# Performance work log

Hardware: AMD Instinct MI355X
Metric: run time of the kernel (lower is better)

## Reference

```python
import jax, jax.numpy as jnp
import numpy as np

HEADS = 8
CPH = 32


def _rel_pos_indices(h, w):
    # same construction as the torch buffer, done statically in numpy
    coords = np.stack(np.meshgrid(np.arange(h), np.arange(w), indexing='ij')).reshape(2, -1)  # [2, N]
    rel = coords[:, :, None] - coords[:, None, :]  # [2, N, N]
    idx = (rel[0] + h - 1) * (2 * w - 1) + (rel[1] + w - 1)  # [N, N]
    return jnp.asarray(idx, dtype=jnp.int32)


def setup_inputs() -> dict:
    key = jax.random.key(0)
    ks = jax.random.split(key, 6)
    B, C, H, W = 2, 256, 48, 48
    emb = HEADS * CPH  # 256
    x = jax.random.normal(ks[0], (B, C, H, W), dtype=jnp.float32)
    # GDN params (kept positive so sqrt is well-defined)
    gdn_beta = jnp.ones((C,), dtype=jnp.float32)
    gdn_gamma = 0.1 * jnp.eye(C, dtype=jnp.float32) + 0.001 * jax.random.uniform(ks[1], (C, C), dtype=jnp.float32)
    w_qkv = 0.02 * jax.random.normal(ks[2], (3 * emb, C), dtype=jnp.float32)
    w_out = 0.02 * jax.random.normal(ks[3], (C, emb), dtype=jnp.float32)
    b_out = jnp.zeros((C,), dtype=jnp.float32)
    table_size = (2 * H - 1) * (2 * W - 1)
    rel_bias_table = 0.02 * jax.random.normal(ks[4], (table_size, HEADS), dtype=jnp.float32)
    return {"x": x, "gdn_beta": gdn_beta, "gdn_gamma": gdn_gamma,
            "w_qkv": w_qkv, "w_out": w_out, "b_out": b_out,
            "rel_bias_table": rel_bias_table}


def reference(x, gdn_beta, gdn_gamma, w_qkv, w_out, b_out, rel_bias_table):
    B, C, H, W = x.shape
    N = H * W
    emb = HEADS * CPH
    scale = CPH ** (-0.5)

    # GDN: y = x / sqrt(beta + gamma * x^2)  (1x1 conv over channels of x^2)
    norm = jnp.einsum('bchw,dc->bdhw', x * x, gdn_gamma) + gdn_beta[None, :, None, None]
    xn = x / jnp.sqrt(norm)

    # flatten spatial, channels last: [B, N, C]
    t = xn.reshape(B, C, N).transpose(0, 2, 1)

    # qkv projection (no bias)
    qkv = (t @ w_qkv.T).reshape(B, N, 3, HEADS, CPH).transpose(2, 0, 3, 1, 4)  # [3, B, h, N, d]
    q, k, v = qkv[0], qkv[1], qkv[2]

    attn = jnp.einsum('bhnd,bhmd->bhnm', q, k) * scale  # [B, h, N, N]

    # gathered relative position bias: [h, N, N]
    idx = _rel_pos_indices(H, W)  # [N, N], static ints
    bias = rel_bias_table[idx.reshape(-1)].reshape(N, N, HEADS).transpose(2, 0, 1)
    attn = jax.nn.softmax(attn + bias[None], axis=-1)

    # NOTE: faithful to the original quirk — reshape (B, h, N, d) directly
    # to (B, N, C) with NO head/seq transpose, exactly like the torch code.
    res = jnp.einsum('bhnm,bhmd->bhnd', attn, v).reshape(B, N, emb)

    out = res @ w_out.T + b_out  # [B, N, C]
    return out.transpose(0, 2, 1).reshape(B, C, H, W)
```

## Files before the change

kernel.cpp:

```cpp
#include <hip/hip_runtime.h>
#include <cstdint>
#include <cstddef>

typedef __attribute__((ext_vector_type(8))) short short8;
typedef __attribute__((ext_vector_type(4))) float floatx4;
typedef __attribute__((ext_vector_type(4))) unsigned short ushort4v;

#define NB 2
#define NPIX 2304
#define TBL 9025
#define TBLP 9032
#define L2E 1.4426950408889634f
#define QSCALE 0.17677669529663689f

__device__ __forceinline__ float b2f(unsigned short u) {
  union { unsigned int i; float f; } v; v.i = ((unsigned int)u) << 16; return v.f;
}
__device__ __forceinline__ unsigned short f2b(float f) {
  union { float f; unsigned int i; } v; v.f = f;
  return (unsigned short)((v.i + 0x7fffu + ((v.i >> 16) & 1u)) >> 16);
}
__device__ __forceinline__ unsigned short f2b_fast(float f) {
  union { float f; unsigned int i; } v; v.f = f;
  return (unsigned short)((v.i + 0x8000u) >> 16);
}

__global__ __launch_bounds__(256) void prep_k(
    const float* __restrict__ gamma, const float* __restrict__ wqkv,
    const float* __restrict__ wout, const float* __restrict__ table,
    unsigned short* __restrict__ gb, unsigned short* __restrict__ qb,
    unsigned short* __restrict__ wb, float* __restrict__ tbf)
{
  int i = blockIdx.x * 256 + threadIdx.x;
  if (i < 65536)  gb[i] = f2b(gamma[i]);
  if (i < 196608) qb[i] = f2b(wqkv[i]);
  if (i < 65536)  wb[i] = f2b(wout[i]);
  if (i < TBL * 8) {
    int e = i >> 3, h = i & 7;
    tbf[(size_t)h * TBLP + e] = table[i] * L2E;
  }
}

template<int MODE>
__global__ __launch_bounds__(256) void gemm_k(
    const unsigned short* __restrict__ A,
    const void* __restrict__ Bv,
    const float* __restrict__ vec,
    unsigned short* __restrict__ o0,
    unsigned short* __restrict__ o1,
    unsigned short* __restrict__ o2,
    float* __restrict__ of)
{
  __shared__ unsigned short Al[64][40];
  __shared__ unsigned short Bl[64][40];
  const float* __restrict__ X = (const float*)Bv;
  const unsigned short* __restrict__ Bw = (const unsigned short*)Bv;

  const int n0 = blockIdx.x * 64;
  const int m0 = blockIdx.y * 64;
  const int b  = blockIdx.z;
  const int tid = threadIdx.x;
  const int wave = tid >> 6, lane = tid & 63;
  const int wm = wave >> 1, wn = wave & 1;
  const int lm = lane & 15, quad = lane >> 4;

  floatx4 acc[2][2] = {};

  for (int k0 = 0; k0 < 256; k0 += 32) {
    __syncthreads();
    {
      int ml = tid >> 2, ko = (tid & 3) * 8;
      *(short8*)&Al[ml][ko] = *(const short8*)&A[(size_t)(m0 + ml) * 256 + k0 + ko];
    }
    if (MODE == 0) {
      int kk = tid >> 3, n8 = (tid & 7) * 8;
      const float* xr = &X[((size_t)(b * 256 + k0 + kk)) * NPIX + n0 + n8];
      float4 x0 = *(const float4*)xr;
      float4 x1 = *(const float4*)(xr + 4);
      Bl[n8 + 0][kk] = f2b(x0.x * x0.x);
      Bl[n8 + 1][kk] = f2b(x0.y * x0.y);
      Bl[n8 + 2][kk] = f2b(x0.z * x0.z);
      Bl[n8 + 3][kk] = f2b(x0.w * x0.w);
      Bl[n8 + 4][kk] = f2b(x1.x * x1.x);
      Bl[n8 + 5][kk] = f2b(x1.y * x1.y);
      Bl[n8 + 6][kk] = f2b(x1.z * x1.z);
      Bl[n8 + 7][kk] = f2b(x1.w * x1.w);
    } else {
      int nl = tid >> 2, ko = (tid & 3) * 8;
      short8 bv = *(const short8*)&Bw[((size_t)b * NPIX + n0 + nl) * 256 + k0 + ko];
      *(short8*)&Bl[nl][ko] = bv;
    }
    __syncthreads();
    short8 af[2], bfr[2];
    #pragma unroll
    for (int tm = 0; tm < 2; ++tm)
      af[tm] = *(const short8*)&Al[wm*32 + tm*16 + lm][quad*8];
    #pragma unroll
    for (int tn = 0; tn < 2; ++tn)
      bfr[tn] = *(const short8*)&Bl[wn*32 + tn*16 + lm][quad*8];
    #pragma unroll
    for (int tm = 0; tm < 2; ++tm)
      #pragma unroll
      for (int tn = 0; tn < 2; ++tn)
        acc[tm][tn] = __builtin_amdgcn_mfma_f32_16x16x32_bf16(af[tm], bfr[tn], acc[tm][tn], 0, 0, 0);
  }

  #pragma unroll
  for (int tm = 0; tm < 2; ++tm) {
    const int rbase = m0 + wm*32 + tm*16 + quad*4;
    #pragma unroll
    for (int tn = 0; tn < 2; ++tn) {
      const int col = n0 + wn*32 + tn*16 + lm;
      floatx4 a4 = acc[tm][tn];
      if (MODE == 0) {
        ushort4v pk;
        #pragma unroll
        for (int r = 0; r < 4; ++r) {
          int d = rbase + r;
          float xv = X[((size_t)(b * 256 + d)) * NPIX + col];
          pk[r] = f2b(xv * rsqrtf(vec[d] + a4[r]));
        }
        *(ushort4v*)&o0[((size_t)(b * NPIX + col)) * 256 + rbase] = pk;
      } else if (MODE == 1) {
        const int part = rbase >> 8, h = (rbase >> 5) & 7, dd = rbase & 31;
        if (part == 2) {
          #pragma unroll
          for (int r = 0; r < 4; ++r)
            o2[(((size_t)(b * 8 + h)) * 32 + dd + r) * NPIX + col] = f2b(a4[r]);
        } else {
          unsigned short* dst = part == 0 ? o0 : o1;
          const float sc = (part == 0) ? (QSCALE * L2E) : 1.0f;
          ushort4v pk;
          #pragma unroll
          for (int r = 0; r < 4; ++r) pk[r] = f2b(a4[r] * sc);
          *(ushort4v*)&dst[(((size_t)(b * 8 + h)) * NPIX + col) * 32 + dd] = pk;
        }
      } else {
        #pragma unroll
        for (int r = 0; r < 4; ++r) {
          int c = rbase + r;
          of[((size_t)(b * 256 + c)) * NPIX + col] = a4[r] + vec[c];
        }
      }
    }
  }
}

__global__ __launch_bounds__(256) void attn_k(
    const unsigned short* __restrict__ qg, const unsigned short* __restrict__ kg,
    const unsigned short* __restrict__ vt, const float* __restrict__ tabf_g,
    unsigned short* __restrict__ ob)
{
  __shared__ __align__(16) float tabf[TBLP];
  __shared__ __align__(16) unsigned short Pl[4][16][72];

  const int tid = threadIdx.x;
  const int w = tid >> 6, lane = tid & 63;
  const int lm = lane & 15, quad = lane >> 4;
  const int q0 = blockIdx.x * 64;
  const int bh = blockIdx.y;
  const size_t base = (size_t)bh * NPIX * 32;

  {
    const float* src = tabf_g + (size_t)(bh & 7) * TBLP;
    for (int e = tid * 4; e < TBLP; e += 1024)
      *(float4*)&tabf[e] = *(const float4*)&src[e];
  }
  __syncthreads();

  const int q = q0 + w * 16 + lm;
  const short8 qfrag = *(const short8*)&qg[base + (size_t)q * 32 + quad * 8];

  const int hi = (q * 43691) >> 21;
  const int rb = (hi + 47) * 95 + (q - hi * 48) + 47;

  float lsum = 0.f;
  floatx4 o[2] = {};

  for (int t = 0; t < 36; ++t) {
    const int j0 = t * 64;
    floatx4 s4[4];
    #pragma unroll
    for (int kt = 0; kt < 4; ++kt) {
      short8 kf = *(const short8*)&kg[base + (size_t)(j0 + kt * 16 + lm) * 32 + quad * 8];
      floatx4 z = {};
      s4[kt] = __builtin_amdgcn_mfma_f32_16x16x32_bf16(kf, qfrag, z, 0, 0, 0);
    }
    #pragma unroll
    for (int kt = 0; kt < 4; ++kt) {
      const int key0 = j0 + kt * 16 + quad * 4;
      const int hj = (key0 * 43691) >> 21;
      const int ib = rb - key0 - hj * 47;
      ushort4v pk;
      #pragma unroll
      for (int r = 0; r < 4; ++r) {
        float p = __builtin_amdgcn_exp2f(s4[kt][r] + tabf[ib - r]);
        lsum += p;
        pk[r] = f2b_fast(p);
      }
      *(ushort4v*)&Pl[w][lm][kt * 16 + quad * 4] = pk;
    }
    __asm__ volatile("s_waitcnt lgkmcnt(0)" ::: "memory");
    #pragma unroll
    for (int c = 0; c < 2; ++c) {
      short8 pf = *(const short8*)&Pl[w][lm][c * 32 + quad * 8];
      #pragma unroll
      for (int dt = 0; dt < 2; ++dt) {
        short8 vf = *(const short8*)&vt[base + (size_t)(dt * 16 + lm) * NPIX + j0 + c * 32 + quad * 8];
        o[dt] = __builtin_amdgcn_mfma_f32_16x16x32_bf16(vf, pf, o[dt], 0, 0, 0);
      }
    }
  }

  lsum += __shfl_xor(lsum, 16, 64);
  lsum += __shfl_xor(lsum, 32, 64);
  const float inv = 1.f / lsum;

  #pragma unroll
  for (int dt = 0; dt < 2; ++dt) {
    ushort4v pk;
    #pragma unroll
    for (int r = 0; r < 4; ++r) pk[r] = f2b(o[dt][r] * inv);
    *(ushort4v*)&ob[base + (size_t)q * 32 + dt * 16 + quad * 4] = pk;
  }
}

extern "C" void kernel_launch(void* const* d_in, const int* in_sizes, int n_in,
                              void* d_out, int out_size, void* d_ws, size_t ws_size,
                              hipStream_t stream) {
  const float* x     = (const float*)d_in[0];
  const float* beta  = (const float*)d_in[1];
  const float* gamma = (const float*)d_in[2];
  const float* wqkv  = (const float*)d_in[3];
  const float* wout  = (const float*)d_in[4];
  const float* bout  = (const float*)d_in[5];
  const float* table = (const float*)d_in[6];
  float* out = (float*)d_out;

  unsigned short* ws = (unsigned short*)d_ws;
  const size_t NE = (size_t)NB * NPIX * 256;
  unsigned short* xn_t  = ws;
  unsigned short* qbuf  = ws + NE;
  unsigned short* kbuf  = ws + 2 * NE;
  unsigned short* vtbuf = ws + 3 * NE;
  unsigned short* obuf  = ws + 4 * NE;
  unsigned short* gam_b = obuf;
  unsigned short* qkv_b = obuf + 65536;
  unsigned short* out_b = ws + 5 * NE;
  float* tab_f = (float*)(ws + 5 * NE + 65536);

  prep_k<<<768, 256, 0, stream>>>(gamma, wqkv, wout, table, gam_b, qkv_b, out_b, tab_f);
  gemm_k<0><<<dim3(36, 4, 2), 256, 0, stream>>>(gam_b, x, beta, xn_t, nullptr, nullptr, nullptr);
  gemm_k<1><<<dim3(36, 12, 2), 256, 0, stream>>>(qkv_b, xn_t, nullptr, qbuf, kbuf, vtbuf, nullptr);
  attn_k<<<dim3(36, 16), 256, 0, stream>>>(qbuf, kbuf, vtbuf, tab_f, obuf);
  gemm_k<2><<<dim3(36, 4, 2), 256, 0, stream>>>(out_b, obuf, bout, nullptr, nullptr, nullptr, out);
}
```

Before: 169.4 us.

## Split attention key range across two wave groups and prefetch K/V registers

The attention block grows to 512 threads. Two groups of four waves each process half of the key sequence for the same 64 queries, and their partial outputs and row sums are combined through shared memory at the end. K and V fragments for the next tile are loaded into registers while the current tile is computed, to hide global load latency. This doubles the waves per block and adds a final reduction and barrier. It also raises register pressure from the prefetch buffers.

New measurement: 169.2 us. Within noise of the previous version (-0.1%).

```diff
diff --git a/kernel.cpp b/kernel.cpp
--- a/kernel.cpp
+++ b/kernel.cpp
@@ -146,29 +146,32 @@
   }
 }
 
-__global__ __launch_bounds__(256) void attn_k(
+__global__ __launch_bounds__(512, 4) void attn_k(
     const unsigned short* __restrict__ qg, const unsigned short* __restrict__ kg,
     const unsigned short* __restrict__ vt, const float* __restrict__ tabf_g,
     unsigned short* __restrict__ ob)
 {
   __shared__ __align__(16) float tabf[TBLP];
-  __shared__ __align__(16) unsigned short Pl[4][16][72];
+  __shared__ __align__(16) unsigned short Pl[8][16][72];
+  __shared__ float lpart[2][4][16];
 
   const int tid = threadIdx.x;
   const int w = tid >> 6, lane = tid & 63;
   const int lm = lane & 15, quad = lane >> 4;
+  const int gq = w & 3, half = w >> 2;
   const int q0 = blockIdx.x * 64;
   const int bh = blockIdx.y;
   const size_t base = (size_t)bh * NPIX * 32;
+  const int j00 = half * 1152;
 
   {
     const float* src = tabf_g + (size_t)(bh & 7) * TBLP;
-    for (int e = tid * 4; e < TBLP; e += 1024)
+    for (int e = tid * 4; e < TBLP; e += 2048)
       *(float4*)&tabf[e] = *(const float4*)&src[e];
   }
   __syncthreads();
 
-  const int q = q0 + w * 16 + lm;
+  const int q = q0 + gq * 16 + lm;
   const short8 qfrag = *(const short8*)&qg[base + (size_t)q * 32 + quad * 8];
 
   const int hi = (q * 43691) >> 21;
@@ -177,14 +180,34 @@
   float lsum = 0.f;
   floatx4 o[2] = {};
 
-  for (int t = 0; t < 36; ++t) {
-    const int j0 = t * 64;
+  short8 kf[4], vf[4];
+  #pragma unroll
+  for (int kt = 0; kt < 4; ++kt)
+    kf[kt] = *(const short8*)&kg[base + (size_t)(j00 + kt * 16 + lm) * 32 + quad * 8];
+  #pragma unroll
+  for (int c = 0; c < 2; ++c)
+    #pragma unroll
+    for (int dt = 0; dt < 2; ++dt)
+      vf[c * 2 + dt] = *(const short8*)&vt[base + (size_t)(dt * 16 + lm) * NPIX + j00 + c * 32 + quad * 8];
+
+  for (int t = 0; t < 18; ++t) {
+    const int j0 = j00 + t * 64;
+    const int j0n = j00 + (t < 17 ? t + 1 : t) * 64;
+    short8 kn[4], vn[4];
+    #pragma unroll
+    for (int kt = 0; kt < 4; ++kt)
+      kn[kt] = *(const short8*)&kg[base + (size_t)(j0n + kt * 16 + lm) * 32 + quad * 8];
+    #pragma unroll
+    for (int c = 0; c < 2; ++c)
+      #pragma unroll
+      for (int dt = 0; dt < 2; ++dt)
+        vn[c * 2 + dt] = *(const short8*)&vt[base + (size_t)(dt * 16 + lm) * NPIX + j0n + c * 32 + quad * 8];
+
     floatx4 s4[4];
     #pragma unroll
     for (int kt = 0; kt < 4; ++kt) {
-      short8 kf = *(const short8*)&kg[base + (size_t)(j0 + kt * 16 + lm) * 32 + quad * 8];
       floatx4 z = {};
-      s4[kt] = __builtin_amdgcn_mfma_f32_16x16x32_bf16(kf, qfrag, z, 0, 0, 0);
+      s4[kt] = __builtin_amdgcn_mfma_f32_16x16x32_bf16(kf[kt], qfrag, z, 0, 0, 0);
     }
     #pragma unroll
     for (int kt = 0; kt < 4; ++kt) {
@@ -205,23 +228,36 @@
     for (int c = 0; c < 2; ++c) {
       short8 pf = *(const short8*)&Pl[w][lm][c * 32 + quad * 8];
       #pragma unroll
-      for (int dt = 0; dt < 2; ++dt) {
-        short8 vf = *(const short8*)&vt[base + (size_t)(dt * 16 + lm) * NPIX + j0 + c * 32 + quad * 8];
-        o[dt] = __builtin_amdgcn_mfma_f32_16x16x32_bf16(vf, pf, o[dt], 0, 0, 0);
-      }
-    }
+      for (int dt = 0; dt < 2; ++dt)
+        o[dt] = __builtin_amdgcn_mfma_f32_16x16x32_bf16(vf[c * 2 + dt], pf, o[dt], 0, 0, 0);
+    }
+    #pragma unroll
+    for (int i2 = 0; i2 < 4; ++i2) { kf[i2] = kn[i2]; vf[i2] = vn[i2]; }
   }
 
   lsum += __shfl_xor(lsum, 16, 64);
   lsum += __shfl_xor(lsum, 32, 64);
-  const float inv = 1.f / lsum;
-
-  #pragma unroll
-  for (int dt = 0; dt < 2; ++dt) {
-    ushort4v pk;
-    #pragma unroll
-    for (int r = 0; r < 4; ++r) pk[r] = f2b(o[dt][r] * inv);
-    *(ushort4v*)&ob[base + (size_t)q * 32 + dt * 16 + quad * 4] = pk;
+
+  float* Om = (float*)&Pl[0][0][0];
+  {
+    const int rowb = ((half * 4 + gq) * 16 + lm) * 36;
+    #pragma unroll
+    for (int dt = 0; dt < 2; ++dt)
+      *(floatx4*)&Om[rowb + dt * 16 + quad * 4] = o[dt];
+    if (quad == 0) lpart[half][gq][lm] = lsum;
+  }
+  __syncthreads();
+
+  if (w < 4) {
+    const int qq = lane >> 2, dg = lane & 3;
+    const float inv = 1.f / (lpart[0][w][qq] + lpart[1][w][qq]);
+    const float* r0 = &Om[((0 * 4 + w) * 16 + qq) * 36 + dg * 8];
+    const float* r1 = &Om[((1 * 4 + w) * 16 + qq) * 36 + dg * 8];
+    short8 pk;
+    #pragma unroll
+    for (int r = 0; r < 8; ++r)
+      pk[r] = (short)f2b((r0[r] + r1[r]) * inv);
+    *(short8*)&ob[base + (size_t)(q0 + w * 16 + qq) * 32 + dg * 8] = pk;
   }
 }
 
@@ -252,6 +288,6 @@
   prep_k<<<768, 256, 0, stream>>>(gamma, wqkv, wout, table, gam_b, qkv_b, out_b, tab_f);
   gemm_k<0><<<dim3(36, 4, 2), 256, 0, stream>>>(gam_b, x, beta, xn_t, nullptr, nullptr, nullptr);
   gemm_k<1><<<dim3(36, 12, 2), 256, 0, stream>>>(qkv_b, xn_t, nullptr, qbuf, kbuf, vtbuf, nullptr);
-  attn_k<<<dim3(36, 16), 256, 0, stream>>>(qbuf, kbuf, vtbuf, tab_f, obuf);
+  attn_k<<<dim3(36, 16), 512, 0, stream>>>(qbuf, kbuf, vtbuf, tab_f, obuf);
   gemm_k<2><<<dim3(36, 4, 2), 256, 0, stream>>>(out_b, obuf, bout, nullptr, nullptr, nullptr, out);
 }
```

## Split attention keys across two wave groups, shuffle P in registers, remap grid

Applied to the files above, without the earlier changes.

The attention kernel now runs 512-thread blocks in which two halves of the waves each process half of the key range for the same 64 queries. Partial outputs and row sums are combined through shared memory at the end. The probability tile is now passed to the PV MFMA operand layout with cross-lane shuffles of packed bf16 pairs instead of an LDS round-trip. The block index is also remapped so that consecutive blocks cover different heads. The goals are more parallel work per query block, fewer LDS stalls and more latency hiding, at the cost of extra shuffles, a final reduction and a block-wide sync.

Result: no change. 172.0 us (+1.5%).

```diff
diff --git a/kernel.cpp b/kernel.cpp
--- a/kernel.cpp
+++ b/kernel.cpp
@@ -20,9 +20,9 @@
   union { float f; unsigned int i; } v; v.f = f;
   return (unsigned short)((v.i + 0x7fffu + ((v.i >> 16) & 1u)) >> 16);
 }
-__device__ __forceinline__ unsigned short f2b_fast(float f) {
-  union { float f; unsigned int i; } v; v.f = f;
-  return (unsigned short)((v.i + 0x8000u) >> 16);
+__device__ __forceinline__ unsigned int f2b2_fast(float lo, float hi) {
+  union { float f; unsigned int i; } a, b; a.f = lo; b.f = hi;
+  return ((a.i + 0x8000u) >> 16) | (((b.i + 0x8000u) >> 16) << 16);
 }
 
 __global__ __launch_bounds__(256) void prep_k(
@@ -146,29 +146,33 @@
   }
 }
 
-__global__ __launch_bounds__(256) void attn_k(
+__global__ __launch_bounds__(512, 4) void attn_k(
     const unsigned short* __restrict__ qg, const unsigned short* __restrict__ kg,
     const unsigned short* __restrict__ vt, const float* __restrict__ tabf_g,
     unsigned short* __restrict__ ob)
 {
   __shared__ __align__(16) float tabf[TBLP];
-  __shared__ __align__(16) unsigned short Pl[4][16][72];
+  __shared__ __align__(16) float Om[8][16][36];
+  __shared__ float lpart[2][4][16];
 
   const int tid = threadIdx.x;
   const int w = tid >> 6, lane = tid & 63;
   const int lm = lane & 15, quad = lane >> 4;
-  const int q0 = blockIdx.x * 64;
-  const int bh = blockIdx.y;
+  const int gq = w & 3, half = w >> 2;
+  const int bi = blockIdx.x;
+  const int bh = (bi & 7) + 8 * ((bi >> 3) & 1);
+  const int q0 = (bi >> 4) * 64;
   const size_t base = (size_t)bh * NPIX * 32;
+  const int j00 = half * 1152;
 
   {
     const float* src = tabf_g + (size_t)(bh & 7) * TBLP;
-    for (int e = tid * 4; e < TBLP; e += 1024)
+    for (int e = tid * 4; e < TBLP; e += 2048)
       *(float4*)&tabf[e] = *(const float4*)&src[e];
   }
   __syncthreads();
 
-  const int q = q0 + w * 16 + lm;
+  const int q = q0 + gq * 16 + lm;
   const short8 qfrag = *(const short8*)&qg[base + (size_t)q * 32 + quad * 8];
 
   const int hi = (q * 43691) >> 21;
@@ -177,8 +181,12 @@
   float lsum = 0.f;
   floatx4 o[2] = {};
 
-  for (int t = 0; t < 36; ++t) {
-    const int j0 = t * 64;
+  const int sA = lm + 16 * (2 * (quad & 1));
+  const int ktsel = quad >> 1;
+
+  for (int t = 0; t < 18; ++t) {
+    const int j0 = j00 + t * 64;
+
     floatx4 s4[4];
     #pragma unroll
     for (int kt = 0; kt < 4; ++kt) {
@@ -186,24 +194,32 @@
       floatx4 z = {};
       s4[kt] = __builtin_amdgcn_mfma_f32_16x16x32_bf16(kf, qfrag, z, 0, 0, 0);
     }
+    unsigned int pp[4][2];
     #pragma unroll
     for (int kt = 0; kt < 4; ++kt) {
       const int key0 = j0 + kt * 16 + quad * 4;
       const int hj = (key0 * 43691) >> 21;
       const int ib = rb - key0 - hj * 47;
-      ushort4v pk;
+      float p0 = __builtin_amdgcn_exp2f(s4[kt][0] + tabf[ib]);
+      float p1 = __builtin_amdgcn_exp2f(s4[kt][1] + tabf[ib - 1]);
+      float p2 = __builtin_amdgcn_exp2f(s4[kt][2] + tabf[ib - 2]);
+      float p3 = __builtin_amdgcn_exp2f(s4[kt][3] + tabf[ib - 3]);
+      lsum += (p0 + p1) + (p2 + p3);
+      pp[kt][0] = f2b2_fast(p0, p1);
+      pp[kt][1] = f2b2_fast(p2, p3);
+    }
+    #pragma unroll
+    for (int c = 0; c < 2; ++c) {
+      short8 pf;
       #pragma unroll
-      for (int r = 0; r < 4; ++r) {
-        float p = __builtin_amdgcn_exp2f(s4[kt][r] + tabf[ib - r]);
-        lsum += p;
-        pk[r] = f2b_fast(p);
+      for (int g = 0; g < 4; ++g) {
+        const int sl = sA + 16 * (g >> 1);
+        unsigned int u0 = (unsigned int)__shfl((int)pp[2 * c + 0][g & 1], sl, 64);
+        unsigned int u1 = (unsigned int)__shfl((int)pp[2 * c + 1][g & 1], sl, 64);
+        unsigned int u = ktsel ? u1 : u0;
+        pf[2 * g]     = (short)(u & 0xffffu);
+        pf[2 * g + 1] = (short)(u >> 16);
       }
-      *(ushort4v*)&Pl[w][lm][kt * 16 + quad * 4] = pk;
-    }
-    __asm__ volatile("s_waitcnt lgkmcnt(0)" ::: "memory");
-    #pragma unroll
-    for (int c = 0; c < 2; ++c) {
-      short8 pf = *(const short8*)&Pl[w][lm][c * 32 + quad * 8];
       #pragma unroll
       for (int dt = 0; dt < 2; ++dt) {
         short8 vf = *(const short8*)&vt[base + (size_t)(dt * 16 + lm) * NPIX + j0 + c * 32 + quad * 8];
@@ -214,14 +230,26 @@
 
   lsum += __shfl_xor(lsum, 16, 64);
   lsum += __shfl_xor(lsum, 32, 64);
-  const float inv = 1.f / lsum;
-
-  #pragma unroll
-  for (int dt = 0; dt < 2; ++dt) {
-    ushort4v pk;
-    #pragma unroll
-    for (int r = 0; r < 4; ++r) pk[r] = f2b(o[dt][r] * inv);
-    *(ushort4v*)&ob[base + (size_t)q * 32 + dt * 16 + quad * 4] = pk;
+
+  {
+    const int row = half * 4 + gq;
+    #pragma unroll
+    for (int dt = 0; dt < 2; ++dt)
+      *(floatx4*)&Om[row][lm][dt * 16 + quad * 4] = o[dt];
+    if (quad == 0) lpart[half][gq][lm] = lsum;
+  }
+  __syncthreads();
+
+  if (w < 4) {
+    const int qq = lane >> 2, dg = lane & 3;
+    const float inv = 1.f / (lpart[0][w][qq] + lpart[1][w][qq]);
+    const float* r0 = &Om[w][qq][dg * 8];
+    const float* r1 = &Om[4 + w][qq][dg * 8];
+    short8 pk;
+    #pragma unroll
+    for (int r = 0; r < 8; ++r)
+      pk[r] = (short)f2b((r0[r] + r1[r]) * inv);
+    *(short8*)&ob[base + (size_t)(q0 + w * 16 + qq) * 32 + dg * 8] = pk;
   }
 }
 
@@ -252,6 +280,6 @@
   prep_k<<<768, 256, 0, stream>>>(gamma, wqkv, wout, table, gam_b, qkv_b, out_b, tab_f);
   gemm_k<0><<<dim3(36, 4, 2), 256, 0, stream>>>(gam_b, x, beta, xn_t, nullptr, nullptr, nullptr);
   gemm_k<1><<<dim3(36, 12, 2), 256, 0, stream>>>(qkv_b, xn_t, nullptr, qbuf, kbuf, vtbuf, nullptr);
-  attn_k<<<dim3(36, 16), 256, 0, stream>>>(qbuf, kbuf, vtbuf, tab_f, obuf);
+  attn_k<<<576, 512, 0, stream>>>(qbuf, kbuf, vtbuf, tab_f, obuf);
   gemm_k<2><<<dim3(36, 4, 2), 256, 0, stream>>>(out_b, obuf, bout, nullptr, nullptr, nullptr, out);
 }
```
